# Kernel tuning notes

Measured on AMD Instinct MI355X. Metric: run time of the kernel, lower is better.

## Reference

```python
import jax, jax.numpy as jnp
import numpy as np

N, E, EQ, DIM = 50000, 800000, 100000, 256


def setup_inputs() -> dict:
    key = jax.random.key(0)
    k1, k2, k3, k4, k5 = jax.random.split(key, 5)
    edges = jax.random.randint(k1, (2, EQ), 0, N)
    adj_row = jax.random.randint(k2, (E,), 0, N)
    adj_col = jax.random.randint(k3, (E,), 0, N)
    node_weight = jax.random.uniform(k4, (N,), dtype=jnp.float32)
    # torchhd-style bipolar hypervectors scaled by sqrt(1/dim)
    scale = (1.0 / DIM) ** 0.5
    node_vectors = jnp.sign(jax.random.normal(k5, (N, DIM), dtype=jnp.float32)) * scale
    return dict(edges=edges, adj_row=adj_row, adj_col=adj_col,
                node_weight=node_weight, node_vectors=node_vectors)


def reference(edges, adj_row, adj_col, node_weight, node_vectors):
    n = node_vectors.shape[0]
    # get_random_node_vectors: embedding * node_weight
    x = node_vectors * node_weight[:, None]                       # [N, dim]
    # one_hop_x = A @ x ; two_hop_x = A @ one_hop_x (binary adjacency)
    one_hop = jax.ops.segment_sum(x[adj_col], adj_row, num_segments=n)       # [N, dim]
    two_hop = jax.ops.segment_sum(one_hop[adj_col], adj_row, num_segments=n)  # [N, dim]
    deg = jax.ops.segment_sum(jnp.ones(adj_row.shape, x.dtype), adj_row, num_segments=n)  # [N]
    s, t = edges[0], edges[1]
    dot = lambda a, b: (a * b).sum(-1)
    count_1_1 = dot(one_hop[s], one_hop[t])
    count_1_2 = dot(one_hop[s], two_hop[t]) + dot(two_hop[s], one_hop[t])
    count_2_2 = dot(two_hop[s] - deg[s][:, None] * x[s],
                    two_hop[t] - deg[t][:, None] * x[t])
    count_self_1_2 = dot(one_hop[s], two_hop[s]) + dot(one_hop[t], two_hop[t])
    return (count_1_1, count_1_2, count_2_2, count_self_1_2)
```

## Files before the change

### kernel.cpp

```cpp
#include <hip/hip_runtime.h>

#define DIM 256
#define DIM4 (DIM / 4)
#define DIMU2 (DIM / 4)

__device__ __forceinline__ unsigned int f2bf_rne(float f) {
    unsigned int u = __float_as_uint(f);
    return (u + 0x7fffu + ((u >> 16) & 1u)) >> 16;
}
__device__ __forceinline__ float bf_lo(unsigned int u) {
    return __uint_as_float(u << 16);
}
__device__ __forceinline__ float bf_hi(unsigned int u) {
    return __uint_as_float(u & 0xffff0000u);
}
__device__ __forceinline__ uint2 pack4(float a, float b, float c, float d) {
    uint2 r;
    r.x = f2bf_rne(a) | (f2bf_rne(b) << 16);
    r.y = f2bf_rne(c) | (f2bf_rne(d) << 16);
    return r;
}

__global__ void compute_x_kernel(const float* __restrict__ nv,
                                 const float* __restrict__ w,
                                 uint2* __restrict__ xb,
                                 int total4) {
    int i = blockIdx.x * blockDim.x + threadIdx.x;
    int stride = gridDim.x * blockDim.x;
    for (; i < total4; i += stride) {
        float4 v = reinterpret_cast<const float4*>(nv)[i];
        float wt = w[i / DIM4];
        xb[i] = pack4(v.x * wt, v.y * wt, v.z * wt, v.w * wt);
    }
}

__global__ void hist_kernel(const int* __restrict__ row,
                            int* __restrict__ cnt, int nedges) {
    int e = blockIdx.x * blockDim.x + threadIdx.x;
    if (e < nedges) atomicAdd(&cnt[row[e]], 1);
}

__global__ void block_sum_kernel(const int* __restrict__ cnt,
                                 int* __restrict__ sums, int n) {
    __shared__ int lds[256];
    int i = blockIdx.x * 256 + threadIdx.x;
    lds[threadIdx.x] = (i < n) ? cnt[i] : 0;
    __syncthreads();
    #pragma unroll
    for (int off = 128; off > 0; off >>= 1) {
        if (threadIdx.x < off) lds[threadIdx.x] += lds[threadIdx.x + off];
        __syncthreads();
    }
    if (threadIdx.x == 0) sums[blockIdx.x] = lds[0];
}

__global__ void scan_sums_kernel(int* __restrict__ sums, int nb,
                                 int* __restrict__ row_ptr_n) {
    __shared__ int lds[256];
    int v = (threadIdx.x < nb) ? sums[threadIdx.x] : 0;
    lds[threadIdx.x] = v;
    __syncthreads();
    #pragma unroll
    for (int off = 1; off < 256; off <<= 1) {
        int t = (threadIdx.x >= off) ? lds[threadIdx.x - off] : 0;
        __syncthreads();
        lds[threadIdx.x] += t;
        __syncthreads();
    }
    if (threadIdx.x < nb) sums[threadIdx.x] = lds[threadIdx.x] - v;
    if (threadIdx.x == 255) *row_ptr_n = lds[255];
}

__global__ void scan_block_kernel(const int* __restrict__ cnt,
                                  const int* __restrict__ sums,
                                  int* __restrict__ row_ptr,
                                  int* __restrict__ cursor, int n) {
    __shared__ int lds[256];
    int i = blockIdx.x * 256 + threadIdx.x;
    int v = (i < n) ? cnt[i] : 0;
    lds[threadIdx.x] = v;
    __syncthreads();
    #pragma unroll
    for (int off = 1; off < 256; off <<= 1) {
        int t = (threadIdx.x >= off) ? lds[threadIdx.x - off] : 0;
        __syncthreads();
        lds[threadIdx.x] += t;
        __syncthreads();
    }
    if (i < n) {
        int excl = sums[blockIdx.x] + lds[threadIdx.x] - v;
        row_ptr[i] = excl;
        cursor[i] = excl;
    }
}

__global__ void scatter_perm_kernel(const int* __restrict__ row,
                                    const int* __restrict__ col,
                                    int* __restrict__ cursor,
                                    int* __restrict__ perm, int nedges) {
    int e = blockIdx.x * blockDim.x + threadIdx.x;
    if (e < nedges) {
        int pos = atomicAdd(&cursor[row[e]], 1);
        perm[pos] = col[e];
    }
}

__global__ void gather_hop_kernel(const int* __restrict__ row_ptr,
                                  const int* __restrict__ perm,
                                  const uint2* __restrict__ src,
                                  uint2* __restrict__ dst, int n) {
    int gid = blockIdx.x * blockDim.x + threadIdx.x;
    int r = gid >> 6;
    int lane = gid & 63;
    if (r >= n) return;
    int beg = row_ptr[r];
    int end = row_ptr[r + 1];
    float a0 = 0.f, a1 = 0.f, a2 = 0.f, a3 = 0.f;
    int e = beg;
    for (; e + 2 <= end; e += 2) {
        int c0 = perm[e];
        int c1 = perm[e + 1];
        uint2 v0 = src[(size_t)c0 * DIMU2 + lane];
        uint2 v1 = src[(size_t)c1 * DIMU2 + lane];
        a0 += bf_lo(v0.x); a1 += bf_hi(v0.x);
        a2 += bf_lo(v0.y); a3 += bf_hi(v0.y);
        a0 += bf_lo(v1.x); a1 += bf_hi(v1.x);
        a2 += bf_lo(v1.y); a3 += bf_hi(v1.y);
    }
    if (e < end) {
        int c0 = perm[e];
        uint2 v0 = src[(size_t)c0 * DIMU2 + lane];
        a0 += bf_lo(v0.x); a1 += bf_hi(v0.x);
        a2 += bf_lo(v0.y); a3 += bf_hi(v0.y);
    }
    dst[(size_t)r * DIMU2 + lane] = pack4(a0, a1, a2, a3);
}

__global__ void query_kernel(const int* __restrict__ es,
                             const int* __restrict__ et,
                             const uint2* __restrict__ xb,
                             const uint2* __restrict__ ohb,
                             const uint2* __restrict__ thb,
                             const int* __restrict__ row_ptr,
                             float* __restrict__ out, int nq) {
    int gid = blockIdx.x * blockDim.x + threadIdx.x;
    int q = gid >> 6;
    int lane = gid & 63;
    if (q >= nq) return;

    int s = es[q];
    int t = et[q];

    uint2 vxs = xb [(size_t)s * DIMU2 + lane];
    uint2 vxt = xb [(size_t)t * DIMU2 + lane];
    uint2 vos = ohb[(size_t)s * DIMU2 + lane];
    uint2 vot = ohb[(size_t)t * DIMU2 + lane];
    uint2 vts = thb[(size_t)s * DIMU2 + lane];
    uint2 vtt = thb[(size_t)t * DIMU2 + lane];
    float ds = (float)(row_ptr[s + 1] - row_ptr[s]);
    float dt = (float)(row_ptr[t + 1] - row_ptr[t]);

    float c11 = 0.f, c12 = 0.f, c22 = 0.f, cs = 0.f;
    #pragma unroll
    for (int k = 0; k < 4; ++k) {
        float fxs, fxt, fos, fot, fts, ftt;
        switch (k) {
            case 0: fxs = bf_lo(vxs.x); fxt = bf_lo(vxt.x); fos = bf_lo(vos.x);
                    fot = bf_lo(vot.x); fts = bf_lo(vts.x); ftt = bf_lo(vtt.x); break;
            case 1: fxs = bf_hi(vxs.x); fxt = bf_hi(vxt.x); fos = bf_hi(vos.x);
                    fot = bf_hi(vot.x); fts = bf_hi(vts.x); ftt = bf_hi(vtt.x); break;
            case 2: fxs = bf_lo(vxs.y); fxt = bf_lo(vxt.y); fos = bf_lo(vos.y);
                    fot = bf_lo(vot.y); fts = bf_lo(vts.y); ftt = bf_lo(vtt.y); break;
            default:fxs = bf_hi(vxs.y); fxt = bf_hi(vxt.y); fos = bf_hi(vos.y);
                    fot = bf_hi(vot.y); fts = bf_hi(vts.y); ftt = bf_hi(vtt.y); break;
        }
        c11 += fos * fot;
        c12 += fos * ftt + fts * fot;
        float as = fts - ds * fxs;
        float bt = ftt - dt * fxt;
        c22 += as * bt;
        cs  += fos * fts + fot * ftt;
    }

    #pragma unroll
    for (int off = 32; off > 0; off >>= 1) {
        c11 += __shfl_xor(c11, off);
        c12 += __shfl_xor(c12, off);
        c22 += __shfl_xor(c22, off);
        cs  += __shfl_xor(cs,  off);
    }

    if (lane == 0) {
        out[q]          = c11;
        out[nq + q]     = c12;
        out[2 * nq + q] = c22;
        out[3 * nq + q] = cs;
    }
}

extern "C" void kernel_launch(void* const* d_in, const int* in_sizes, int n_in,
                              void* d_out, int out_size, void* d_ws, size_t ws_size,
                              hipStream_t stream) {
    const int*   edges        = (const int*)  d_in[0];
    const int*   adj_row      = (const int*)  d_in[1];
    const int*   adj_col      = (const int*)  d_in[2];
    const float* node_weight  = (const float*)d_in[3];
    const float* node_vectors = (const float*)d_in[4];

    const int EQ = in_sizes[0] / 2;
    const int E  = in_sizes[1];
    const int N  = in_sizes[3];

    uint2* xb  = (uint2*)d_ws;
    uint2* ohb = xb  + (size_t)N * DIMU2;
    uint2* thb = ohb + (size_t)N * DIMU2;
    int* row_ptr = (int*)(thb + (size_t)N * DIMU2);
    int* cursor  = row_ptr + (N + 1);
    int* cnt     = cursor + N;
    int* perm    = cnt + N;
    int* sums    = perm + E;

    const int* es = edges;
    const int* et = edges + EQ;
    float* out = (float*)d_out;

    int nb = (N + 255) / 256;

    hipMemsetAsync(cnt, 0, (size_t)N * sizeof(int), stream);
    hist_kernel<<<(E + 255) / 256, 256, 0, stream>>>(adj_row, cnt, E);
    block_sum_kernel<<<nb, 256, 0, stream>>>(cnt, sums, N);
    scan_sums_kernel<<<1, 256, 0, stream>>>(sums, nb, row_ptr + N);
    scan_block_kernel<<<nb, 256, 0, stream>>>(cnt, sums, row_ptr, cursor, N);
    scatter_perm_kernel<<<(E + 255) / 256, 256, 0, stream>>>(adj_row, adj_col,
                                                             cursor, perm, E);

    int total4 = N * DIM4;
    compute_x_kernel<<<2048, 256, 0, stream>>>(node_vectors, node_weight, xb, total4);

    int gthreads = N * 64;
    int gblocks = (gthreads + 255) / 256;
    gather_hop_kernel<<<gblocks, 256, 0, stream>>>(row_ptr, perm, xb, ohb, N);
    gather_hop_kernel<<<gblocks, 256, 0, stream>>>(row_ptr, perm, ohb, thb, N);

    int qthreads = EQ * 64;
    query_kernel<<<(qthreads + 255) / 256, 256, 0, stream>>>(
        es, et, xb, ohb, thb, row_ptr, out, EQ);
}
```

Measured before the change: 280.8 us.

## Interleave x, one-hop and two-hop rows per node and split gathers across half-waves

Stores x, one-hop and two-hop bf16 vectors contiguously per node in a single 1536-byte record, so each query reads both endpoints from two contiguous regions instead of six scattered rows. The gather kernel now loads 16-byte uint4 per lane, with each half-wave processing alternating edges, and combines the two halves with a cross-lane shuffle before writing. The aim is fewer, wider memory transactions and better locality for the random-access gathers. The cost is a larger stride between rows in the gather source, so each gathered cache line set also holds unrelated slots, plus a shuffle reduction per row.

Result: faster. 271.1 us (-3.5%).

```diff
diff --git a/kernel.cpp b/kernel.cpp
--- a/kernel.cpp
+++ b/kernel.cpp
@@ -1,8 +1,12 @@
 #include <hip/hip_runtime.h>
 
 #define DIM 256
-#define DIM4 (DIM / 4)
-#define DIMU2 (DIM / 4)
+#define NODE_U2 192
+#define NODE_U4 96
+#define SLOT_OH_U2 64
+#define SLOT_TH_U2 128
+#define SLOT_OH_U4 32
+#define SLOT_TH_U4 64
 
 __device__ __forceinline__ unsigned int f2bf_rne(float f) {
     unsigned int u = __float_as_uint(f);
@@ -14,23 +18,25 @@
 __device__ __forceinline__ float bf_hi(unsigned int u) {
     return __uint_as_float(u & 0xffff0000u);
 }
-__device__ __forceinline__ uint2 pack4(float a, float b, float c, float d) {
-    uint2 r;
-    r.x = f2bf_rne(a) | (f2bf_rne(b) << 16);
-    r.y = f2bf_rne(c) | (f2bf_rne(d) << 16);
-    return r;
+__device__ __forceinline__ unsigned int pack2(float a, float b) {
+    return f2bf_rne(a) | (f2bf_rne(b) << 16);
 }
 
 __global__ void compute_x_kernel(const float* __restrict__ nv,
                                  const float* __restrict__ w,
-                                 uint2* __restrict__ xb,
-                                 int total4) {
+                                 uint2* __restrict__ cmb,
+                                 int total_u2) {
     int i = blockIdx.x * blockDim.x + threadIdx.x;
     int stride = gridDim.x * blockDim.x;
-    for (; i < total4; i += stride) {
+    for (; i < total_u2; i += stride) {
         float4 v = reinterpret_cast<const float4*>(nv)[i];
-        float wt = w[i / DIM4];
-        xb[i] = pack4(v.x * wt, v.y * wt, v.z * wt, v.w * wt);
+        int node = i >> 6;
+        int j = i & 63;
+        float wt = w[node];
+        uint2 r;
+        r.x = pack2(v.x * wt, v.y * wt);
+        r.y = pack2(v.z * wt, v.w * wt);
+        cmb[(size_t)node * NODE_U2 + j] = r;
     }
 }
 
@@ -107,56 +113,83 @@
 
 __global__ void gather_hop_kernel(const int* __restrict__ row_ptr,
                                   const int* __restrict__ perm,
-                                  const uint2* __restrict__ src,
-                                  uint2* __restrict__ dst, int n) {
+                                  const uint4* __restrict__ src,
+                                  uint4* __restrict__ dst, int n) {
     int gid = blockIdx.x * blockDim.x + threadIdx.x;
     int r = gid >> 6;
+    if (r >= n) return;
     int lane = gid & 63;
-    if (r >= n) return;
+    int h = lane >> 5;
+    int l = lane & 31;
+
     int beg = row_ptr[r];
     int end = row_ptr[r + 1];
+
     float a0 = 0.f, a1 = 0.f, a2 = 0.f, a3 = 0.f;
-    int e = beg;
-    for (; e + 2 <= end; e += 2) {
+    float a4 = 0.f, a5 = 0.f, a6 = 0.f, a7 = 0.f;
+
+    int e = beg + h;
+    while (e + 2 < end) {
         int c0 = perm[e];
-        int c1 = perm[e + 1];
-        uint2 v0 = src[(size_t)c0 * DIMU2 + lane];
-        uint2 v1 = src[(size_t)c1 * DIMU2 + lane];
+        int c1 = perm[e + 2];
+        uint4 v0 = src[(size_t)c0 * NODE_U4 + l];
+        uint4 v1 = src[(size_t)c1 * NODE_U4 + l];
         a0 += bf_lo(v0.x); a1 += bf_hi(v0.x);
         a2 += bf_lo(v0.y); a3 += bf_hi(v0.y);
+        a4 += bf_lo(v0.z); a5 += bf_hi(v0.z);
+        a6 += bf_lo(v0.w); a7 += bf_hi(v0.w);
         a0 += bf_lo(v1.x); a1 += bf_hi(v1.x);
         a2 += bf_lo(v1.y); a3 += bf_hi(v1.y);
+        a4 += bf_lo(v1.z); a5 += bf_hi(v1.z);
+        a6 += bf_lo(v1.w); a7 += bf_hi(v1.w);
+        e += 4;
     }
     if (e < end) {
         int c0 = perm[e];
-        uint2 v0 = src[(size_t)c0 * DIMU2 + lane];
+        uint4 v0 = src[(size_t)c0 * NODE_U4 + l];
         a0 += bf_lo(v0.x); a1 += bf_hi(v0.x);
         a2 += bf_lo(v0.y); a3 += bf_hi(v0.y);
-    }
-    dst[(size_t)r * DIMU2 + lane] = pack4(a0, a1, a2, a3);
+        a4 += bf_lo(v0.z); a5 += bf_hi(v0.z);
+        a6 += bf_lo(v0.w); a7 += bf_hi(v0.w);
+    }
+
+    a0 += __shfl_xor(a0, 32); a1 += __shfl_xor(a1, 32);
+    a2 += __shfl_xor(a2, 32); a3 += __shfl_xor(a3, 32);
+    a4 += __shfl_xor(a4, 32); a5 += __shfl_xor(a5, 32);
+    a6 += __shfl_xor(a6, 32); a7 += __shfl_xor(a7, 32);
+
+    if (lane < 32) {
+        uint4 o;
+        o.x = pack2(a0, a1);
+        o.y = pack2(a2, a3);
+        o.z = pack2(a4, a5);
+        o.w = pack2(a6, a7);
+        dst[(size_t)r * NODE_U4 + l] = o;
+    }
 }
 
 __global__ void query_kernel(const int* __restrict__ es,
                              const int* __restrict__ et,
-                             const uint2* __restrict__ xb,
-                             const uint2* __restrict__ ohb,
-                             const uint2* __restrict__ thb,
+                             const uint2* __restrict__ cmb,
                              const int* __restrict__ row_ptr,
                              float* __restrict__ out, int nq) {
     int gid = blockIdx.x * blockDim.x + threadIdx.x;
     int q = gid >> 6;
+    if (q >= nq) return;
     int lane = gid & 63;
-    if (q >= nq) return;
 
     int s = es[q];
     int t = et[q];
 
-    uint2 vxs = xb [(size_t)s * DIMU2 + lane];
-    uint2 vxt = xb [(size_t)t * DIMU2 + lane];
-    uint2 vos = ohb[(size_t)s * DIMU2 + lane];
-    uint2 vot = ohb[(size_t)t * DIMU2 + lane];
-    uint2 vts = thb[(size_t)s * DIMU2 + lane];
-    uint2 vtt = thb[(size_t)t * DIMU2 + lane];
+    const uint2* ns = cmb + (size_t)s * NODE_U2;
+    const uint2* nt = cmb + (size_t)t * NODE_U2;
+
+    uint2 vxs = ns[lane];
+    uint2 vos = ns[SLOT_OH_U2 + lane];
+    uint2 vts = ns[SLOT_TH_U2 + lane];
+    uint2 vxt = nt[lane];
+    uint2 vot = nt[SLOT_OH_U2 + lane];
+    uint2 vtt = nt[SLOT_TH_U2 + lane];
     float ds = (float)(row_ptr[s + 1] - row_ptr[s]);
     float dt = (float)(row_ptr[t + 1] - row_ptr[t]);
 
@@ -211,10 +244,8 @@
     const int E  = in_sizes[1];
     const int N  = in_sizes[3];
 
-    uint2* xb  = (uint2*)d_ws;
-    uint2* ohb = xb  + (size_t)N * DIMU2;
-    uint2* thb = ohb + (size_t)N * DIMU2;
-    int* row_ptr = (int*)(thb + (size_t)N * DIMU2);
+    uint2* cmb = (uint2*)d_ws;
+    int* row_ptr = (int*)(cmb + (size_t)N * NODE_U2);
     int* cursor  = row_ptr + (N + 1);
     int* cnt     = cursor + N;
     int* perm    = cnt + N;
@@ -234,15 +265,19 @@
     scatter_perm_kernel<<<(E + 255) / 256, 256, 0, stream>>>(adj_row, adj_col,
                                                              cursor, perm, E);
 
-    int total4 = N * DIM4;
-    compute_x_kernel<<<2048, 256, 0, stream>>>(node_vectors, node_weight, xb, total4);
-
+    int total_u2 = N * 64;
+    compute_x_kernel<<<2048, 256, 0, stream>>>(node_vectors, node_weight, cmb,
+                                               total_u2);
+
+    const uint4* cmb4 = (const uint4*)cmb;
     int gthreads = N * 64;
     int gblocks = (gthreads + 255) / 256;
-    gather_hop_kernel<<<gblocks, 256, 0, stream>>>(row_ptr, perm, xb, ohb, N);
-    gather_hop_kernel<<<gblocks, 256, 0, stream>>>(row_ptr, perm, ohb, thb, N);
+    gather_hop_kernel<<<gblocks, 256, 0, stream>>>(
+        row_ptr, perm, cmb4, (uint4*)cmb4 + SLOT_OH_U4, N);
+    gather_hop_kernel<<<gblocks, 256, 0, stream>>>(
+        row_ptr, perm, cmb4 + SLOT_OH_U4, (uint4*)cmb4 + SLOT_TH_U4, N);
 
     int qthreads = EQ * 64;
     query_kernel<<<(qthreads + 255) / 256, 256, 0, stream>>>(
-        es, et, xb, ohb, thb, row_ptr, out, EQ);
-}
+        es, et, cmb, row_ptr, out, EQ);
+}
```
